# Kernel optimization log

Hardware: AMD Instinct MI355X
Metric: run time of the kernel (lower is better)

Reference implementation:

```python
import jax, jax.numpy as jnp
import numpy as np

N_NODES = 100000
N_EDGES = 640000
D_IN = 128
D_OUT = 128
D_HID = 128  # assumed MLP hidden width (repo MLP not shown; standard 2-layer GIN MLP)


def setup_inputs() -> dict:
    key = jax.random.key(0)
    k = jax.random.split(key, 8)
    x = jax.random.normal(k[0], (N_NODES, D_IN), dtype=jnp.float32)
    edge_index = jax.random.randint(k[1], (2, N_EDGES), 0, N_NODES, dtype=jnp.int64)
    edge_attr = jax.random.normal(k[2], (N_EDGES, D_IN), dtype=jnp.float32)
    # learned params
    eps = jnp.zeros((), dtype=jnp.float32)  # train_eps=True, init 0
    s1 = 1.0 / np.sqrt(D_IN)
    s2 = 1.0 / np.sqrt(D_HID)
    W1 = jax.random.uniform(k[3], (D_IN, D_HID), jnp.float32, -s1, s1)
    b1 = jax.random.uniform(k[4], (D_HID,), jnp.float32, -s1, s1)
    W2 = jax.random.uniform(k[5], (D_HID, D_OUT), jnp.float32, -s2, s2)
    b2 = jax.random.uniform(k[6], (D_OUT,), jnp.float32, -s2, s2)
    return {"x": x, "edge_index": edge_index, "edge_attr": edge_attr,
            "eps": eps, "W1": W1, "b1": b1, "W2": W2, "b2": b2}


def reference(x, edge_index, edge_attr, eps, W1, b1, W2, b2):
    src = edge_index[0]  # source nodes j
    dst = edge_index[1]  # target nodes i
    # message: ReLU(x_j + edge_attr)  -- [E, D_IN]
    msg = jax.nn.relu(x[src] + edge_attr)
    # scatter-sum aggregation to target nodes -- [N, D_IN]
    aggr = jax.ops.segment_sum(msg, dst, num_segments=N_NODES)
    # GINE update: (1 + eps) * x_i + aggr, then MLP (dropout=0.0 -> identity)
    h = (1.0 + eps) * x + aggr
    h = jax.nn.relu(h @ W1 + b1)
    out = h @ W2 + b2
    return out
```

## Files before the change

### kernel.cpp

```cpp
#include <hip/hip_runtime.h>
#include <hip/hip_bf16.h>

constexpr int NN = 100000;
constexpr int NE = 640000;
constexpr int D  = 128;
constexpr int NB = (NN + 255) / 256;

typedef __attribute__((ext_vector_type(8))) short bf16x8;
typedef __attribute__((ext_vector_type(4))) float f32x4;

__device__ __forceinline__ short f2bf(float f) {
    union { float f; unsigned u; } v; v.f = f;
    unsigned r = v.u + 0x7FFF + ((v.u >> 16) & 1);
    return (short)(r >> 16);
}
__device__ __forceinline__ float bf2f(short h) {
    union { unsigned u; float f; } v;
    v.u = ((unsigned)(unsigned short)h) << 16;
    return v.f;
}
__device__ __forceinline__ unsigned cvtpk(float a, float b) {
    union { __hip_bfloat162 h2; unsigned u; } cv;
    float2 f; f.x = a; f.y = b;
    cv.h2 = __float22bfloat162_rn(f);
    return cv.u;
}
__device__ __forceinline__ void pack_hilo(const float* v, bf16x8& hi, bf16x8& lo) {
#pragma unroll
    for (int i = 0; i < 4; ++i) {
        unsigned u = cvtpk(v[2 * i], v[2 * i + 1]);
        short h0 = (short)(u & 0xFFFF), h1 = (short)(u >> 16);
        hi[2 * i] = h0; hi[2 * i + 1] = h1;
        unsigned ul = cvtpk(v[2 * i] - bf2f(h0), v[2 * i + 1] - bf2f(h1));
        lo[2 * i] = (short)(ul & 0xFFFF); lo[2 * i + 1] = (short)(ul >> 16);
    }
}
__device__ __forceinline__ bf16x8 pack_bf8(const float* v) {
    bf16x8 o;
#pragma unroll
    for (int i = 0; i < 4; ++i) {
        unsigned u = cvtpk(v[2 * i], v[2 * i + 1]);
        o[2 * i] = (short)(u & 0xFFFF); o[2 * i + 1] = (short)(u >> 16);
    }
    return o;
}

__global__ __launch_bounds__(256) void k_zero(int* __restrict__ cnt) {
    int i = blockIdx.x * 256 + threadIdx.x;
    if (i < NN) cnt[i] = 0;
}

__global__ __launch_bounds__(256) void k_hist(const int* __restrict__ dst,
                                              int* __restrict__ cnt) {
    int e = blockIdx.x * 256 + threadIdx.x;
    if (e < NE) atomicAdd(&cnt[dst[e]], 1);
}

__global__ __launch_bounds__(256) void k_bsum(const int* __restrict__ cnt,
                                              int* __restrict__ bsum) {
    int i = blockIdx.x * 256 + threadIdx.x;
    int v = (i < NN) ? cnt[i] : 0;
#pragma unroll
    for (int s = 32; s; s >>= 1) v += __shfl_down(v, s, 64);
    __shared__ int w[4];
    if ((threadIdx.x & 63) == 0) w[threadIdx.x >> 6] = v;
    __syncthreads();
    if (threadIdx.x == 0) bsum[blockIdx.x] = w[0] + w[1] + w[2] + w[3];
}

__global__ __launch_bounds__(512) void k_scan_bsum(const int* __restrict__ bsum,
                                                   int* __restrict__ bboff) {
    int t = threadIdx.x, lane = t & 63;
    int v = (t < NB) ? bsum[t] : 0;
    int incl = v;
#pragma unroll
    for (int s = 1; s < 64; s <<= 1) {
        int u = __shfl_up(incl, s, 64);
        if (lane >= s) incl += u;
    }
    __shared__ int wt[8], wp[8];
    if (lane == 63) wt[t >> 6] = incl;
    __syncthreads();
    if (t == 0) { int run = 0; for (int i = 0; i < 8; ++i) { wp[i] = run; run += wt[i]; } }
    __syncthreads();
    if (t < NB) bboff[t] = incl - v + wp[t >> 6];
}

__global__ __launch_bounds__(256) void k_scan_final(const int* __restrict__ cnt,
                                                    const int* __restrict__ bboff,
                                                    int* __restrict__ off,
                                                    int* __restrict__ cur) {
    int b = blockIdx.x, t = threadIdx.x, lane = t & 63;
    int i = b * 256 + t;
    int v = (i < NN) ? cnt[i] : 0;
    int incl = v;
#pragma unroll
    for (int s = 1; s < 64; s <<= 1) {
        int u = __shfl_up(incl, s, 64);
        if (lane >= s) incl += u;
    }
    __shared__ int wt[4], wp[4];
    if (lane == 63) wt[t >> 6] = incl;
    __syncthreads();
    if (t == 0) { int run = 0; for (int q = 0; q < 4; ++q) { wp[q] = run; run += wt[q]; } }
    __syncthreads();
    int excl = incl - v + wp[t >> 6] + bboff[b];
    if (i < NN) { off[i] = excl; cur[i] = excl; }
    if (i == 0) off[NN] = NE;
}

__global__ __launch_bounds__(256) void k_perm(const int* __restrict__ dst,
                                              const int* __restrict__ src,
                                              int* __restrict__ cur,
                                              int2* __restrict__ ps) {
    int e = blockIdx.x * 256 + threadIdx.x;
    if (e < NE) {
        int p = atomicAdd(&cur[dst[e]], 1);
        int2 v; v.x = e; v.y = src[e];
        ps[p] = v;
    }
}

__global__ __launch_bounds__(256) void k_wsplit(const float* __restrict__ W,
                                                short* __restrict__ Whi,
                                                short* __restrict__ Wlo) {
    for (int idx = blockIdx.x * 256 + threadIdx.x; idx < D * D; idx += gridDim.x * 256) {
        int n = idx >> 7, k = idx & 127;
        float w = W[k * D + n];
        short hi = f2bf(w);
        Whi[idx] = hi;
        Wlo[idx] = f2bf(w - bf2f(hi));
    }
}

constexpr int LDG = 132;

__global__ __launch_bounds__(256, 8) void k_fused(const float* __restrict__ x,
                                                  const float* __restrict__ ea,
                                                  const int* __restrict__ off,
                                                  const int2* __restrict__ ps,
                                                  const float* __restrict__ eps,
                                                  const short* __restrict__ W1h,
                                                  const short* __restrict__ W1l,
                                                  const short* __restrict__ W2h,
                                                  const short* __restrict__ W2l,
                                                  const float* __restrict__ b1,
                                                  const float* __restrict__ b2,
                                                  float* __restrict__ out) {
    __shared__ float G1[16 * LDG];
    __shared__ float G2[16 * LDG];

    const int wave = threadIdx.x >> 6;
    const int lane = threadIdx.x & 63;
    const int nb = blockIdx.x * 16;

    {
        const int lo2 = lane * 2;
        const float sc = 1.0f + eps[0];
        for (int t = 0; t < 4; ++t) {
            const int n = nb + wave * 4 + t;
            const int j0 = off[n], j1 = off[n + 1];
            float accx = 0.0f, accy = 0.0f;
            for (int j = j0; j < j1; j += 8) {
                int ee[8], ss[8];
#pragma unroll
                for (int q = 0; q < 8; ++q) {
                    int jj = j + q; jj = (jj < j1) ? jj : (j1 - 1);
                    int2 p = ps[jj];
                    ee[q] = p.x; ss[q] = p.y;
                }
                float2 xa[8], eb[8];
#pragma unroll
                for (int q = 0; q < 8; ++q) {
                    xa[q] = *reinterpret_cast<const float2*>(x  + (size_t)ss[q] * D + lo2);
                    eb[q] = *reinterpret_cast<const float2*>(ea + (size_t)ee[q] * D + lo2);
                }
#pragma unroll
                for (int q = 0; q < 8; ++q) {
                    float mx = fmaxf(xa[q].x + eb[q].x, 0.0f);
                    float my = fmaxf(xa[q].y + eb[q].y, 0.0f);
                    bool ok = (j + q) < j1;
                    accx += ok ? mx : 0.0f;
                    accy += ok ? my : 0.0f;
                }
            }
            float2 xx = *reinterpret_cast<const float2*>(x + (size_t)n * D + lo2);
            float2 o;
            o.x = fmaf(sc, xx.x, accx);
            o.y = fmaf(sc, xx.y, accy);
            *reinterpret_cast<float2*>(&G1[(wave * 4 + t) * LDG + lo2]) = o;
        }
    }
    __syncthreads();

    const int r = lane & 15;
    const int g = lane >> 4;

    {
        f32x4 acc[2];
#pragma unroll
        for (int nl = 0; nl < 2; ++nl) {
            acc[nl].x = 0.f; acc[nl].y = 0.f; acc[nl].z = 0.f; acc[nl].w = 0.f;
        }

#pragma unroll
        for (int kc = 0; kc < 4; ++kc) {
            const int k0 = kc * 32;
            bf16x8 ahi, alo;
            {
                const float* gp = &G1[r * LDG + k0 + g * 8];
                float vals[8];
                *reinterpret_cast<float4*>(&vals[0]) = reinterpret_cast<const float4*>(gp)[0];
                *reinterpret_cast<float4*>(&vals[4]) = reinterpret_cast<const float4*>(gp)[1];
                pack_hilo(vals, ahi, alo);
            }
#pragma unroll
            for (int nl = 0; nl < 2; ++nl) {
                const int nt = wave * 2 + nl;
                const int wb = (nt * 16 + r) * D + k0 + g * 8;
                bf16x8 whi = *reinterpret_cast<const bf16x8*>(&W1h[wb]);
                bf16x8 wlo = *reinterpret_cast<const bf16x8*>(&W1l[wb]);
                acc[nl] = __builtin_amdgcn_mfma_f32_16x16x32_bf16(ahi, whi, acc[nl], 0, 0, 0);
                acc[nl] = __builtin_amdgcn_mfma_f32_16x16x32_bf16(ahi, wlo, acc[nl], 0, 0, 0);
                acc[nl] = __builtin_amdgcn_mfma_f32_16x16x32_bf16(alo, whi, acc[nl], 0, 0, 0);
            }
        }

#pragma unroll
        for (int nl = 0; nl < 2; ++nl) {
            const int col = (wave * 2 + nl) * 16 + r;
            const float bb = b1[col];
#pragma unroll
            for (int q = 0; q < 4; ++q)
                G2[(g * 4 + q) * LDG + col] = fmaxf(acc[nl][q] + bb, 0.0f);
        }
    }
    __syncthreads();

    {
        f32x4 acc[2];
#pragma unroll
        for (int nl = 0; nl < 2; ++nl) {
            acc[nl].x = 0.f; acc[nl].y = 0.f; acc[nl].z = 0.f; acc[nl].w = 0.f;
        }

#pragma unroll
        for (int kc = 0; kc < 4; ++kc) {
            const int k0 = kc * 32;
            bf16x8 a;
            {
                const float* gp = &G2[r * LDG + k0 + g * 8];
                float vals[8];
                *reinterpret_cast<float4*>(&vals[0]) = reinterpret_cast<const float4*>(gp)[0];
                *reinterpret_cast<float4*>(&vals[4]) = reinterpret_cast<const float4*>(gp)[1];
                a = pack_bf8(vals);
            }
#pragma unroll
            for (int nl = 0; nl < 2; ++nl) {
                const int nt = wave * 2 + nl;
                const int wb = (nt * 16 + r) * D + k0 + g * 8;
                bf16x8 whi = *reinterpret_cast<const bf16x8*>(&W2h[wb]);
                bf16x8 wlo = *reinterpret_cast<const bf16x8*>(&W2l[wb]);
                acc[nl] = __builtin_amdgcn_mfma_f32_16x16x32_bf16(a, whi, acc[nl], 0, 0, 0);
                acc[nl] = __builtin_amdgcn_mfma_f32_16x16x32_bf16(a, wlo, acc[nl], 0, 0, 0);
            }
        }

#pragma unroll
        for (int nl = 0; nl < 2; ++nl) {
            const int col = (wave * 2 + nl) * 16 + r;
            const float bb = b2[col];
#pragma unroll
            for (int q = 0; q < 4; ++q) {
                long row = nb + g * 4 + q;
                out[row * D + col] = acc[nl][q] + bb;
            }
        }
    }
}

extern "C" void kernel_launch(void* const* d_in, const int* in_sizes, int n_in,
                              void* d_out, int out_size, void* d_ws, size_t ws_size,
                              hipStream_t stream) {
    const float* x   = (const float*)d_in[0];
    const int*   ei  = (const int*)d_in[1];
    const float* ea  = (const float*)d_in[2];
    const float* eps = (const float*)d_in[3];
    const float* W1  = (const float*)d_in[4];
    const float* b1  = (const float*)d_in[5];
    const float* W2  = (const float*)d_in[6];
    const float* b2  = (const float*)d_in[7];
    float* out = (float*)d_out;

    const int* src = ei;
    const int* dst = ei + NE;

    int* base  = (int*)d_ws;
    int* cnt   = base;
    int* off   = cnt + NN;
    int* cur   = off + NN + 1;
    int* bsum  = cur + NN;
    int* bboff = bsum + NB;
    size_t ps_off = ((size_t)(3 * NN + 1 + 2 * NB) + 1) & ~(size_t)1;
    int2* ps   = (int2*)(base + ps_off);
    short* wsp = (short*)(base + ps_off + 2 * (size_t)NE);
    short* W1h = wsp;
    short* W1l = W1h + D * D;
    short* W2h = W1l + D * D;
    short* W2l = W2h + D * D;

    k_wsplit    <<<32,               256, 0, stream>>>(W1, W1h, W1l);
    k_wsplit    <<<32,               256, 0, stream>>>(W2, W2h, W2l);
    k_zero      <<<NB,               256, 0, stream>>>(cnt);
    k_hist      <<<(NE + 255) / 256, 256, 0, stream>>>(dst, cnt);
    k_bsum      <<<NB,               256, 0, stream>>>(cnt, bsum);
    k_scan_bsum <<<1,                512, 0, stream>>>(bsum, bboff);
    k_scan_final<<<NB,               256, 0, stream>>>(cnt, bboff, off, cur);
    k_perm      <<<(NE + 255) / 256, 256, 0, stream>>>(dst, src, cur, ps);

    k_fused<<<NN / 16, 256, 0, stream>>>(x, ea, off, ps, eps,
                                         W1h, W1l, W2h, W2l, b1, b2, out);
}
```

Before: 306.6 us.

## Give each wave its own 16-node tile and merge weight split kernels

Result: slower. 321.4 us (+4.8%).

```diff
diff --git a/kernel.cpp b/kernel.cpp
--- a/kernel.cpp
+++ b/kernel.cpp
@@ -121,44 +121,53 @@
     }
 }
 
-__global__ __launch_bounds__(256) void k_wsplit(const float* __restrict__ W,
-                                                short* __restrict__ Whi,
-                                                short* __restrict__ Wlo) {
-    for (int idx = blockIdx.x * 256 + threadIdx.x; idx < D * D; idx += gridDim.x * 256) {
+__global__ __launch_bounds__(256) void k_wsplit2(const float* __restrict__ W1,
+                                                 const float* __restrict__ W2,
+                                                 short* __restrict__ W1h,
+                                                 short* __restrict__ W1l,
+                                                 short* __restrict__ W2h,
+                                                 short* __restrict__ W2l) {
+    for (int t = blockIdx.x * 256 + threadIdx.x; t < 2 * D * D; t += gridDim.x * 256) {
+        int which = t >= D * D;
+        int idx = t - which * D * D;
         int n = idx >> 7, k = idx & 127;
+        const float* W = which ? W2 : W1;
         float w = W[k * D + n];
         short hi = f2bf(w);
-        Whi[idx] = hi;
-        Wlo[idx] = f2bf(w - bf2f(hi));
+        short lo = f2bf(w - bf2f(hi));
+        if (which) { W2h[idx] = hi; W2l[idx] = lo; }
+        else       { W1h[idx] = hi; W1l[idx] = lo; }
     }
 }
 
 constexpr int LDG = 132;
 
-__global__ __launch_bounds__(256, 8) void k_fused(const float* __restrict__ x,
-                                                  const float* __restrict__ ea,
-                                                  const int* __restrict__ off,
-                                                  const int2* __restrict__ ps,
-                                                  const float* __restrict__ eps,
-                                                  const short* __restrict__ W1h,
-                                                  const short* __restrict__ W1l,
-                                                  const short* __restrict__ W2h,
-                                                  const short* __restrict__ W2l,
-                                                  const float* __restrict__ b1,
-                                                  const float* __restrict__ b2,
-                                                  float* __restrict__ out) {
-    __shared__ float G1[16 * LDG];
-    __shared__ float G2[16 * LDG];
+__global__ __launch_bounds__(256) void k_fused(const float* __restrict__ x,
+                                               const float* __restrict__ ea,
+                                               const int* __restrict__ off,
+                                               const int2* __restrict__ ps,
+                                               const float* __restrict__ eps,
+                                               const short* __restrict__ W1h,
+                                               const short* __restrict__ W1l,
+                                               const short* __restrict__ W2h,
+                                               const short* __restrict__ W2l,
+                                               const float* __restrict__ b1,
+                                               const float* __restrict__ b2,
+                                               float* __restrict__ out) {
+    __shared__ float G[4][16 * LDG];
 
     const int wave = threadIdx.x >> 6;
     const int lane = threadIdx.x & 63;
-    const int nb = blockIdx.x * 16;
+    const int n0 = blockIdx.x * 64 + wave * 16;
+    if (n0 >= NN) return;
+
+    float* Gw = G[wave];
 
     {
         const int lo2 = lane * 2;
         const float sc = 1.0f + eps[0];
-        for (int t = 0; t < 4; ++t) {
-            const int n = nb + wave * 4 + t;
+        for (int t = 0; t < 16; ++t) {
+            const int n = n0 + t;
             const int j0 = off[n], j1 = off[n + 1];
             float accx = 0.0f, accy = 0.0f;
             for (int j = j0; j < j1; j += 8) {
@@ -188,19 +197,18 @@
             float2 o;
             o.x = fmaf(sc, xx.x, accx);
             o.y = fmaf(sc, xx.y, accy);
-            *reinterpret_cast<float2*>(&G1[(wave * 4 + t) * LDG + lo2]) = o;
-        }
-    }
-    __syncthreads();
+            *reinterpret_cast<float2*>(&Gw[t * LDG + lo2]) = o;
+        }
+    }
 
     const int r = lane & 15;
     const int g = lane >> 4;
 
     {
-        f32x4 acc[2];
-#pragma unroll
-        for (int nl = 0; nl < 2; ++nl) {
-            acc[nl].x = 0.f; acc[nl].y = 0.f; acc[nl].z = 0.f; acc[nl].w = 0.f;
+        f32x4 acc[8];
+#pragma unroll
+        for (int nt = 0; nt < 8; ++nt) {
+            acc[nt].x = 0.f; acc[nt].y = 0.f; acc[nt].z = 0.f; acc[nt].w = 0.f;
         }
 
 #pragma unroll
@@ -208,40 +216,38 @@
             const int k0 = kc * 32;
             bf16x8 ahi, alo;
             {
-                const float* gp = &G1[r * LDG + k0 + g * 8];
+                const float* gp = &Gw[r * LDG + k0 + g * 8];
                 float vals[8];
                 *reinterpret_cast<float4*>(&vals[0]) = reinterpret_cast<const float4*>(gp)[0];
                 *reinterpret_cast<float4*>(&vals[4]) = reinterpret_cast<const float4*>(gp)[1];
                 pack_hilo(vals, ahi, alo);
             }
 #pragma unroll
-            for (int nl = 0; nl < 2; ++nl) {
-                const int nt = wave * 2 + nl;
+            for (int nt = 0; nt < 8; ++nt) {
                 const int wb = (nt * 16 + r) * D + k0 + g * 8;
                 bf16x8 whi = *reinterpret_cast<const bf16x8*>(&W1h[wb]);
                 bf16x8 wlo = *reinterpret_cast<const bf16x8*>(&W1l[wb]);
-                acc[nl] = __builtin_amdgcn_mfma_f32_16x16x32_bf16(ahi, whi, acc[nl], 0, 0, 0);
-                acc[nl] = __builtin_amdgcn_mfma_f32_16x16x32_bf16(ahi, wlo, acc[nl], 0, 0, 0);
-                acc[nl] = __builtin_amdgcn_mfma_f32_16x16x32_bf16(alo, whi, acc[nl], 0, 0, 0);
-            }
-        }
-
-#pragma unroll
-        for (int nl = 0; nl < 2; ++nl) {
-            const int col = (wave * 2 + nl) * 16 + r;
+                acc[nt] = __builtin_amdgcn_mfma_f32_16x16x32_bf16(ahi, whi, acc[nt], 0, 0, 0);
+                acc[nt] = __builtin_amdgcn_mfma_f32_16x16x32_bf16(ahi, wlo, acc[nt], 0, 0, 0);
+                acc[nt] = __builtin_amdgcn_mfma_f32_16x16x32_bf16(alo, whi, acc[nt], 0, 0, 0);
+            }
+        }
+
+#pragma unroll
+        for (int nt = 0; nt < 8; ++nt) {
+            const int col = nt * 16 + r;
             const float bb = b1[col];
 #pragma unroll
             for (int q = 0; q < 4; ++q)
-                G2[(g * 4 + q) * LDG + col] = fmaxf(acc[nl][q] + bb, 0.0f);
-        }
-    }
-    __syncthreads();
+                Gw[(g * 4 + q) * LDG + col] = fmaxf(acc[nt][q] + bb, 0.0f);
+        }
+    }
 
     {
-        f32x4 acc[2];
-#pragma unroll
-        for (int nl = 0; nl < 2; ++nl) {
-            acc[nl].x = 0.f; acc[nl].y = 0.f; acc[nl].z = 0.f; acc[nl].w = 0.f;
+        f32x4 acc[8];
+#pragma unroll
+        for (int nt = 0; nt < 8; ++nt) {
+            acc[nt].x = 0.f; acc[nt].y = 0.f; acc[nt].z = 0.f; acc[nt].w = 0.f;
         }
 
 #pragma unroll
@@ -249,31 +255,30 @@
             const int k0 = kc * 32;
             bf16x8 a;
             {
-                const float* gp = &G2[r * LDG + k0 + g * 8];
+                const float* gp = &Gw[r * LDG + k0 + g * 8];
                 float vals[8];
                 *reinterpret_cast<float4*>(&vals[0]) = reinterpret_cast<const float4*>(gp)[0];
                 *reinterpret_cast<float4*>(&vals[4]) = reinterpret_cast<const float4*>(gp)[1];
                 a = pack_bf8(vals);
             }
 #pragma unroll
-            for (int nl = 0; nl < 2; ++nl) {
-                const int nt = wave * 2 + nl;
+            for (int nt = 0; nt < 8; ++nt) {
                 const int wb = (nt * 16 + r) * D + k0 + g * 8;
                 bf16x8 whi = *reinterpret_cast<const bf16x8*>(&W2h[wb]);
                 bf16x8 wlo = *reinterpret_cast<const bf16x8*>(&W2l[wb]);
-                acc[nl] = __builtin_amdgcn_mfma_f32_16x16x32_bf16(a, whi, acc[nl], 0, 0, 0);
-                acc[nl] = __builtin_amdgcn_mfma_f32_16x16x32_bf16(a, wlo, acc[nl], 0, 0, 0);
-            }
-        }
-
-#pragma unroll
-        for (int nl = 0; nl < 2; ++nl) {
-            const int col = (wave * 2 + nl) * 16 + r;
+                acc[nt] = __builtin_amdgcn_mfma_f32_16x16x32_bf16(a, whi, acc[nt], 0, 0, 0);
+                acc[nt] = __builtin_amdgcn_mfma_f32_16x16x32_bf16(a, wlo, acc[nt], 0, 0, 0);
+            }
+        }
+
+#pragma unroll
+        for (int nt = 0; nt < 8; ++nt) {
+            const int col = nt * 16 + r;
             const float bb = b2[col];
 #pragma unroll
             for (int q = 0; q < 4; ++q) {
-                long row = nb + g * 4 + q;
-                out[row * D + col] = acc[nl][q] + bb;
+                long row = n0 + g * 4 + q;
+                out[row * D + col] = acc[nt][q] + bb;
             }
         }
     }
@@ -309,8 +314,7 @@
     short* W2h = W1l + D * D;
     short* W2l = W2h + D * D;
 
-    k_wsplit    <<<32,               256, 0, stream>>>(W1, W1h, W1l);
-    k_wsplit    <<<32,               256, 0, stream>>>(W2, W2h, W2l);
+    k_wsplit2   <<<64,               256, 0, stream>>>(W1, W2, W1h, W1l, W2h, W2l);
     k_zero      <<<NB,               256, 0, stream>>>(cnt);
     k_hist      <<<(NE + 255) / 256, 256, 0, stream>>>(dst, cnt);
     k_bsum      <<<NB,               256, 0, stream>>>(cnt, bsum);
@@ -318,6 +322,6 @@
     k_scan_final<<<NB,               256, 0, stream>>>(cnt, bboff, off, cur);
     k_perm      <<<(NE + 255) / 256, 256, 0, stream>>>(dst, src, cur, ps);
 
-    k_fused<<<NN / 16, 256, 0, stream>>>(x, ea, off, ps, eps,
-                                         W1h, W1l, W2h, W2l, b1, b2, out);
-}
+    k_fused<<<(NN + 63) / 64, 256, 0, stream>>>(x, ea, off, ps, eps,
+                                                W1h, W1l, W2h, W2l, b1, b2, out);
+}
```
